# Performance work log

Measured on AMD Instinct MI355X. Metric: run time of the kernel, lower is better.

## Reference

```python
import jax, jax.numpy as jnp
import numpy as np

H = 1024


def _linear(x, W, b):
    # torch nn.Linear: y = x @ W.T + b
    return jnp.einsum('...i,oi->...o', x, W) + b


def setup_inputs() -> dict:
    key = jax.random.key(0)
    ks = jax.random.split(key, 10)
    s = 1.0 / np.sqrt(H)
    inp = {
        'p': jax.random.normal(ks[0], (8, 4096, H), dtype=jnp.float32),
        'x': jax.random.normal(ks[1], (8, 64, H), dtype=jnp.float32),
        'Wq': jax.random.uniform(ks[2], (H, H), jnp.float32, -s, s),
        'bq': jax.random.uniform(ks[3], (H,), jnp.float32, -s, s),
        'Wk': jax.random.uniform(ks[4], (H, H), jnp.float32, -s, s),
        'bk': jax.random.uniform(ks[5], (H,), jnp.float32, -s, s),
        'Wv': jax.random.uniform(ks[6], (H, H), jnp.float32, -s, s),
        'bv': jax.random.uniform(ks[7], (H,), jnp.float32, -s, s),
        'Wg': jax.random.uniform(ks[8], (1, 2 * H), jnp.float32, -s, s),
        'bg': jax.random.uniform(ks[9], (1,), jnp.float32, -s, s),
    }
    return inp


def reference(p, x, Wq, bq, Wk, bk, Wv, bv, Wg, bg):
    q = _linear(p, Wq, bq)            # (B, S, H)
    k = _linear(x, Wk, bk)            # (B, L, H)
    v = _linear(x, Wv, bv)            # (B, L, H)
    # NOTE: scale applied AFTER softmax, faithful to the original module
    scores = jax.nn.softmax(jnp.einsum('bsh,blh->bsl', q, k), axis=-1)
    scores = scores / jnp.sqrt(jnp.asarray(H, p.dtype))
    out = jnp.einsum('bsl,blh->bsh', scores, v) + p
    g = jax.nn.sigmoid(_linear(jnp.concatenate([out, p], axis=2), Wg, bg))  # (B,S,1)
    return g * out + (1.0 - g) * p
```

## Files before the change

kernel.cpp:

```cpp
#include <hip/hip_runtime.h>

#define H 1024
#define SEQ 4096

typedef float f32x4 __attribute__((ext_vector_type(4)));
typedef short s16x8 __attribute__((ext_vector_type(8)));
typedef unsigned short u16;
typedef u16 u16x4 __attribute__((ext_vector_type(4)));
typedef u16 u16x8 __attribute__((ext_vector_type(8)));

__device__ inline u16 f2bf(float f) {
  union { float f; unsigned u; } v; v.f = f;
  unsigned r = v.u + 0x7fffu + ((v.u >> 16) & 1u);
  return (u16)(r >> 16);
}
__device__ inline float bf2f(u16 b) {
  union { unsigned u; float f; } v; v.u = ((unsigned)b) << 16; return v.f;
}

__device__ __forceinline__ void cvt16(const float* __restrict__ src, u16* __restrict__ dst, int i) {
  const float4* s = reinterpret_cast<const float4*>(src) + (size_t)i * 4;
  float4 a = s[0], b = s[1], c = s[2], d = s[3];
  u16x8 lo, hi;
  lo[0]=f2bf(a.x); lo[1]=f2bf(a.y); lo[2]=f2bf(a.z); lo[3]=f2bf(a.w);
  lo[4]=f2bf(b.x); lo[5]=f2bf(b.y); lo[6]=f2bf(b.z); lo[7]=f2bf(b.w);
  hi[0]=f2bf(c.x); hi[1]=f2bf(c.y); hi[2]=f2bf(c.z); hi[3]=f2bf(c.w);
  hi[4]=f2bf(d.x); hi[5]=f2bf(d.y); hi[6]=f2bf(d.z); hi[7]=f2bf(d.w);
  u16x8* o = reinterpret_cast<u16x8*>(dst) + (size_t)i * 2;
  o[0] = lo; o[1] = hi;
}

__global__ __launch_bounds__(256) void prep_kernel(
    const float* __restrict__ Wq, const float* __restrict__ Wk,
    const float* __restrict__ Wv, const float* __restrict__ x,
    const float* __restrict__ Wg,
    u16* __restrict__ wqTb, u16* __restrict__ wkb, u16* __restrict__ wvb,
    u16* __restrict__ xb, float* __restrict__ wgs, float* __restrict__ zeros) {
  __shared__ u16 tls[64][65];
  int blk = blockIdx.x, t = threadIdx.x;
  if (blk < 256) {
    int ti = blk >> 4, tj = blk & 15;
    int lr = t >> 2, cq = (t & 3) * 16;
    const float* s = Wq + (size_t)(ti * 64 + lr) * H + tj * 64 + cq;
#pragma unroll
    for (int q = 0; q < 4; ++q) {
      float4 v = *reinterpret_cast<const float4*>(s + q * 4);
      tls[lr][cq + q * 4 + 0] = f2bf(v.x);
      tls[lr][cq + q * 4 + 1] = f2bf(v.y);
      tls[lr][cq + q * 4 + 2] = f2bf(v.z);
      tls[lr][cq + q * 4 + 3] = f2bf(v.w);
    }
    __syncthreads();
    u16x8 a, b2;
#pragma unroll
    for (int i = 0; i < 8; ++i) a[i] = tls[cq + i][lr];
#pragma unroll
    for (int i = 0; i < 8; ++i) b2[i] = tls[cq + 8 + i][lr];
    u16* d = wqTb + (size_t)(tj * 64 + lr) * H + ti * 64 + cq;
    *reinterpret_cast<u16x8*>(d) = a;
    *reinterpret_cast<u16x8*>(d + 8) = b2;
  } else if (blk < 512) {
    cvt16(Wk, wkb, (blk - 256) * 256 + t);
  } else if (blk < 768) {
    cvt16(Wv, wvb, (blk - 512) * 256 + t);
  } else if (blk < 896) {
    cvt16(x, xb, (blk - 768) * 256 + t);
  } else {
    int i = t * 4;
    float4 a = *reinterpret_cast<const float4*>(Wg + i);
    float4 b2 = *reinterpret_cast<const float4*>(Wg + H + i);
    float4 o; o.x=a.x+b2.x; o.y=a.y+b2.y; o.z=a.z+b2.z; o.w=a.w+b2.w;
    *reinterpret_cast<float4*>(wgs + i) = o;
    float4 z; z.x=0.f; z.y=0.f; z.z=0.f; z.w=0.f;
    *reinterpret_cast<float4*>(zeros + i) = z;
  }
}

__device__ __forceinline__ void gemm_body(const u16* __restrict__ A, const u16* __restrict__ W,
                                          const float* __restrict__ bias, u16* __restrict__ out,
                                          int mt, int nt, int omode, u16* sm) {
  int m0 = mt * 128, n0 = nt * 128;
  int t = threadIdx.x;
  int wave = t >> 6, lane = t & 63;
  int lane15 = lane & 15, lhi = lane >> 4;
  int wr = wave >> 1, wc = wave & 1;
  u16* a_sm = sm;
  u16* b_sm = sm + 8192;

  f32x4 acc[4][4];
#pragma unroll
  for (int mi = 0; mi < 4; ++mi)
#pragma unroll
    for (int ni = 0; ni < 4; ++ni) acc[mi][ni] = (f32x4)0.f;

  int rsel = wave * 32 + (lane >> 3);
  int csel = (lane & 7) * 8;
  const u16* Ab = A + (size_t)m0 * H + csel;
  const u16* Wb = W + (size_t)n0 * H + csel;

  for (int kt = 0; kt < 16; ++kt) {
    int kc = kt * 64;
#pragma unroll
    for (int j = 0; j < 4; ++j) {
      const u16* ga = Ab + (size_t)(rsel + j * 8) * H + kc;
      const u16* gb = Wb + (size_t)(rsel + j * 8) * H + kc;
      __builtin_amdgcn_global_load_lds((const __attribute__((address_space(1))) unsigned int*)ga,
                                       (__attribute__((address_space(3))) unsigned int*)&a_sm[wave * 2048 + j * 512],
                                       16, 0, 0);
      __builtin_amdgcn_global_load_lds((const __attribute__((address_space(1))) unsigned int*)gb,
                                       (__attribute__((address_space(3))) unsigned int*)&b_sm[wave * 2048 + j * 512],
                                       16, 0, 0);
    }
    __syncthreads();
#pragma unroll
    for (int ks = 0; ks < 2; ++ks) {
      s16x8 af[4], bfr[4];
#pragma unroll
      for (int mi = 0; mi < 4; ++mi)
        af[mi] = *reinterpret_cast<const s16x8*>(&a_sm[(wr * 64 + mi * 16 + lane15) * 64 + ks * 32 + lhi * 8]);
#pragma unroll
      for (int ni = 0; ni < 4; ++ni)
        bfr[ni] = *reinterpret_cast<const s16x8*>(&b_sm[(wc * 64 + ni * 16 + lane15) * 64 + ks * 32 + lhi * 8]);
#pragma unroll
      for (int mi = 0; mi < 4; ++mi)
#pragma unroll
        for (int ni = 0; ni < 4; ++ni)
          acc[mi][ni] = __builtin_amdgcn_mfma_f32_16x16x32_bf16(af[mi], bfr[ni], acc[mi][ni], 0, 0, 0);
    }
    __syncthreads();
  }

  float bqv[4];
#pragma unroll
  for (int ni = 0; ni < 4; ++ni) bqv[ni] = bias[n0 + wc * 64 + ni * 16 + lane15];

  if (omode == 0) {
#pragma unroll
    for (int mi = 0; mi < 4; ++mi)
#pragma unroll
      for (int ni = 0; ni < 4; ++ni)
#pragma unroll
        for (int r = 0; r < 4; ++r)
          sm[(wr * 64 + mi * 16 + lhi * 4 + r) * 128 + wc * 64 + ni * 16 + lane15] =
              f2bf(acc[mi][ni][r] + bqv[ni]);
    __syncthreads();
#pragma unroll
    for (int i = 0; i < 4; ++i) {
      int lin2 = i * 4096 + t * 16;
      int row = lin2 >> 7, col = lin2 & 127;
      u16x8 v0 = *reinterpret_cast<const u16x8*>(&sm[lin2]);
      u16x8 v1 = *reinterpret_cast<const u16x8*>(&sm[lin2 + 8]);
      u16* o = out + (size_t)(m0 + row) * H + n0 + col;
      *reinterpret_cast<u16x8*>(o) = v0;
      *reinterpret_cast<u16x8*>(o + 8) = v1;
    }
  } else {
#pragma unroll
    for (int mi = 0; mi < 4; ++mi)
#pragma unroll
      for (int ni = 0; ni < 4; ++ni) {
        int col = n0 + wc * 64 + ni * 16 + lane15;
#pragma unroll
        for (int r = 0; r < 4; ++r) {
          int row = m0 + wr * 64 + mi * 16 + lhi * 4 + r;
          out[((size_t)(row >> 6) * H + col) * 64 + (row & 63)] = f2bf(acc[mi][ni][r] + bqv[ni]);
        }
      }
  }
}

__global__ __launch_bounds__(256) void kv1_kernel(const u16* __restrict__ xb,
                                                  const u16* __restrict__ wkb, const u16* __restrict__ wvb,
                                                  const float* __restrict__ bk, const float* __restrict__ bv,
                                                  u16* __restrict__ kbf, u16* __restrict__ vTb) {
  __shared__ __align__(16) u16 sm[128 * 128];
  int sel = blockIdx.x >> 5;
  int bid = blockIdx.x & 31;
  if (sel == 0)
    gemm_body(xb, wkb, bk, kbf, bid >> 3, bid & 7, 0, sm);
  else
    gemm_body(xb, wvb, bv, vTb, bid >> 3, bid & 7, 2, sm);
}

__global__ __launch_bounds__(256) void kv2_kernel(const u16* __restrict__ kbf,
                                                  const u16* __restrict__ wqTb,
                                                  const float* __restrict__ zeros,
                                                  u16* __restrict__ ktb,
                                                  const u16* __restrict__ vTb,
                                                  const float* __restrict__ Wg,
                                                  const float* __restrict__ bq,
                                                  float* __restrict__ vg, float* __restrict__ bqk) {
  if (blockIdx.x < 32) {
    __shared__ __align__(16) u16 sm[128 * 128];
    gemm_body(kbf, wqTb, zeros, ktb, blockIdx.x >> 3, blockIdx.x & 7, 0, sm);
  } else {
    __shared__ float bq_s[H];
    __shared__ float partial[4][64];
    int b = blockIdx.x - 32, t = threadIdx.x;
    *reinterpret_cast<float4*>(&bq_s[t * 4]) = *reinterpret_cast<const float4*>(bq + t * 4);
    int l = t & 63, part = t >> 6;
    float s = 0.f;
    const u16* vtp = vTb + ((size_t)b * H + part * 256) * 64 + l;
    for (int h = 0; h < 256; ++h) s += bf2f(vtp[h * 64]) * Wg[part * 256 + h];
    partial[part][l] = s;
    __syncthreads();
    if (t < 64) vg[b * 64 + t] = partial[0][t] + partial[1][t] + partial[2][t] + partial[3][t];
    int row = t >> 2, qp = t & 3;
    const u16* kr = kbf + ((size_t)b * 64 + row) * H + qp * 256;
    float sb = 0.f;
    for (int j = 0; j < 256; j += 8) {
      u16x8 v8 = *reinterpret_cast<const u16x8*>(kr + j);
      const float* bqp = &bq_s[qp * 256 + j];
#pragma unroll
      for (int i2 = 0; i2 < 8; ++i2) sb += bf2f(v8[i2]) * bqp[i2];
    }
    sb += __shfl_xor(sb, 1);
    sb += __shfl_xor(sb, 2);
    if (qp == 0) bqk[b * 64 + row] = sb;
  }
}

__global__ __launch_bounds__(128, 2) void attn_kernel(
    const float* __restrict__ p, const u16* __restrict__ ktb,
    const u16* __restrict__ vT, const float* __restrict__ wgs,
    const float* __restrict__ vg, const float* __restrict__ bqk,
    const float* __restrict__ bg, float* __restrict__ out) {
  int t = threadIdx.x;
  int orig = blockIdx.x;
  int lin = (orig & 7) * 128 + (orig >> 3);
  int b = lin >> 7, st = lin & 127;
  size_t gm0 = (size_t)b * SEQ + (size_t)st * 32;
  int wave = t >> 6, lane = t & 63, lane15 = lane & 15, lhi = lane >> 4;

  __shared__ __align__(16) u16 kbuf[3][64 * 64];
  __shared__ __align__(16) u16 pbuf[2][32 * 64];
  __shared__ float wgs_l[H];
  __shared__ float g_l[32], vg_l[64], bq_l[64], pg_l[32];

  *reinterpret_cast<float4*>(&wgs_l[t * 8]) = *reinterpret_cast<const float4*>(wgs + t * 8);
  *reinterpret_cast<float4*>(&wgs_l[t * 8 + 4]) = *reinterpret_cast<const float4*>(wgs + t * 8 + 4);
  if (t < 64) { vg_l[t] = vg[b * 64 + t]; bq_l[t] = bqk[b * 64 + t]; }

  const u16* kb = ktb + (size_t)b * 64 * H;
  int ar = t >> 2, aq = t & 3;
  int awz = (ar & 7) << 3;
  const float* prow = p + (gm0 + ar) * H + aq * 16;
  float pgs = 0.f;

#define KSTAGE(buf, kc)                                                                   \
  {                                                                                       \
    _Pragma("unroll")                                                                     \
    for (int j = 0; j < 4; ++j) {                                                         \
      int row_ = j * 16 + wave * 8 + (lane >> 3);                                         \
      int off_ = (kc) + (((lane & 7) * 8) ^ ((row_ & 7) << 3));                           \
      __builtin_amdgcn_global_load_lds(                                                   \
          (const __attribute__((address_space(1))) unsigned int*)(kb + (size_t)row_ * H + off_), \
          (__attribute__((address_space(3))) unsigned int*)(&kbuf[buf][j * 1024 + wave * 512]),  \
          16, 0, 0);                                                                      \
    }                                                                                     \
  }

#define CVT_WRITE(buf, R, kc)                                                             \
  {                                                                                       \
    const float* w_ = &wgs_l[(kc) + aq * 16];                                             \
    pgs += R[0].x*w_[0]+R[0].y*w_[1]+R[0].z*w_[2]+R[0].w*w_[3]                            \
         + R[1].x*w_[4]+R[1].y*w_[5]+R[1].z*w_[6]+R[1].w*w_[7]                            \
         + R[2].x*w_[8]+R[2].y*w_[9]+R[2].z*w_[10]+R[2].w*w_[11]                          \
         + R[3].x*w_[12]+R[3].y*w_[13]+R[3].z*w_[14]+R[3].w*w_[15];                       \
    u16x8 o0_, o1_;                                                                       \
    o0_[0]=f2bf(R[0].x); o0_[1]=f2bf(R[0].y); o0_[2]=f2bf(R[0].z); o0_[3]=f2bf(R[0].w);   \
    o0_[4]=f2bf(R[1].x); o0_[5]=f2bf(R[1].y); o0_[6]=f2bf(R[1].z); o0_[7]=f2bf(R[1].w);   \
    o1_[0]=f2bf(R[2].x); o1_[1]=f2bf(R[2].y); o1_[2]=f2bf(R[2].z); o1_[3]=f2bf(R[2].w);   \
    o1_[4]=f2bf(R[3].x); o1_[5]=f2bf(R[3].y); o1_[6]=f2bf(R[3].z); o1_[7]=f2bf(R[3].w);   \
    *reinterpret_cast<u16x8*>(&pbuf[buf][ar * 64 + ((aq * 16) ^ awz)]) = o0_;             \
    *reinterpret_cast<u16x8*>(&pbuf[buf][ar * 64 + ((aq * 16 + 8) ^ awz)]) = o1_;         \
  }

#define PLOAD(R, kc)                                                                      \
  {                                                                                       \
    const float* pr_ = prow + (kc);                                                       \
    R[0] = *reinterpret_cast<const float4*>(pr_);                                         \
    R[1] = *reinterpret_cast<const float4*>(pr_ + 4);                                     \
    R[2] = *reinterpret_cast<const float4*>(pr_ + 8);                                     \
    R[3] = *reinterpret_cast<const float4*>(pr_ + 12);                                    \
  }

  float4 rA[4], rB[4], rC[4];
  KSTAGE(0, 0);
  KSTAGE(1, 64);
  PLOAD(rA, 0);
  PLOAD(rB, 64);
  PLOAD(rC, 128);
  __syncthreads();
  CVT_WRITE(0, rA, 0);
  PLOAD(rA, 192);

  f32x4 sacc[4];
#pragma unroll
  for (int ni = 0; ni < 4; ++ni) sacc[ni] = (f32x4)0.f;
  int aswz = (lane15 & 7) << 3;

  for (int kt = 0; kt < 16; ++kt) {
    int cur3 = kt % 3, cur2 = kt & 1;
    if (kt < 14) KSTAGE((kt + 2) % 3, (kt + 2) * 64);
    __builtin_amdgcn_sched_barrier(0);
    if (kt < 15) {
      int sel = (kt + 1) % 3;
      if (sel == 0)      { CVT_WRITE(cur2 ^ 1, rA, (kt + 1) * 64); if (kt < 12) PLOAD(rA, (kt + 4) * 64); }
      else if (sel == 1) { CVT_WRITE(cur2 ^ 1, rB, (kt + 1) * 64); if (kt < 12) PLOAD(rB, (kt + 4) * 64); }
      else               { CVT_WRITE(cur2 ^ 1, rC, (kt + 1) * 64); if (kt < 12) PLOAD(rC, (kt + 4) * 64); }
    }
#pragma unroll
    for (int ks2 = 0; ks2 < 2; ++ks2) {
      int col = ks2 * 32 + lhi * 8;
      s16x8 ap = *reinterpret_cast<const s16x8*>(&pbuf[cur2][(wave * 16 + lane15) * 64 + (col ^ aswz)]);
#pragma unroll
      for (int ni = 0; ni < 4; ++ni) {
        int brow = ni * 16 + lane15;
        s16x8 bk8 = *reinterpret_cast<const s16x8*>(&kbuf[cur3][brow * 64 + (col ^ ((brow & 7) << 3))]);
        sacc[ni] = __builtin_amdgcn_mfma_f32_16x16x32_bf16(ap, bk8, sacc[ni], 0, 0, 0);
      }
    }
    if (kt <= 11) {
      asm volatile("s_waitcnt vmcnt(12)" ::: "memory");
    } else if (kt == 12) {
      asm volatile("s_waitcnt vmcnt(8)" ::: "memory");
    } else {
      asm volatile("s_waitcnt vmcnt(0)" ::: "memory");
    }
    __builtin_amdgcn_s_barrier();
    asm volatile("" ::: "memory");
  }

  pgs += __shfl_xor(pgs, 1);
  pgs += __shfl_xor(pgs, 2);
  if (aq == 0) pg_l[ar] = pgs;
  __syncthreads();

  u16* P_lds = &pbuf[0][0];
  {
    float vgl[4], bql[4];
#pragma unroll
    for (int ni = 0; ni < 4; ++ni) { vgl[ni] = vg_l[ni * 16 + lane15]; bql[ni] = bq_l[ni * 16 + lane15]; }
    float bg0 = bg[0];
#pragma unroll
    for (int r = 0; r < 4; ++r) {
      int row = wave * 16 + lhi * 4 + r;
      float sv[4];
#pragma unroll
      for (int ni = 0; ni < 4; ++ni) sv[ni] = sacc[ni][r] + bql[ni];
      float mx = fmaxf(fmaxf(sv[0], sv[1]), fmaxf(sv[2], sv[3]));
      mx = fmaxf(mx, __shfl_xor(mx, 1));
      mx = fmaxf(mx, __shfl_xor(mx, 2));
      mx = fmaxf(mx, __shfl_xor(mx, 4));
      mx = fmaxf(mx, __shfl_xor(mx, 8));
      float sum = 0.f;
#pragma unroll
      for (int ni = 0; ni < 4; ++ni) {
        float e = __expf(sv[ni] - mx);
        sv[ni] = e;
        sum += e;
      }
      sum += __shfl_xor(sum, 1);
      sum += __shfl_xor(sum, 2);
      sum += __shfl_xor(sum, 4);
      sum += __shfl_xor(sum, 8);
      float inv = 1.f / (32.f * sum);
      float gl = 0.f;
#pragma unroll
      for (int ni = 0; ni < 4; ++ni) {
        float pv = sv[ni] * inv;
        P_lds[row * 72 + ni * 16 + lane15] = f2bf(pv);
        gl += pv * vgl[ni];
      }
      gl += __shfl_xor(gl, 1);
      gl += __shfl_xor(gl, 2);
      gl += __shfl_xor(gl, 4);
      gl += __shfl_xor(gl, 8);
      if (lane15 == 0) {
        float logit = gl + pg_l[row] + bg0;
        g_l[row] = 1.f / (1.f + __expf(-logit));
      }
    }
  }
  __syncthreads();

  {
    s16x8 pa[2][2];
#pragma unroll
    for (int mi = 0; mi < 2; ++mi)
#pragma unroll
      for (int ks = 0; ks < 2; ++ks)
        pa[mi][ks] = *reinterpret_cast<const s16x8*>(&P_lds[(mi * 16 + lane15) * 72 + ks * 32 + lhi * 8]);
    const u16* vb = vT + (size_t)b * H * 64;
    float* sc = reinterpret_cast<float*>(&kbuf[0][0]) + wave * 2048;
    for (int hc = 0; hc < 8; ++hc) {
      int hbase = wave * 512 + hc * 64;
      f32x4 acc[2][4];
#pragma unroll
      for (int mi = 0; mi < 2; ++mi)
#pragma unroll
        for (int ni = 0; ni < 4; ++ni) acc[mi][ni] = (f32x4)0.f;
#pragma unroll
      for (int ks = 0; ks < 2; ++ks) {
        s16x8 bv8[4];
#pragma unroll
        for (int ni = 0; ni < 4; ++ni)
          bv8[ni] = *reinterpret_cast<const s16x8*>(vb + (size_t)(hbase + ni * 16 + lane15) * 64 + ks * 32 + lhi * 8);
#pragma unroll
        for (int mi = 0; mi < 2; ++mi)
#pragma unroll
          for (int ni = 0; ni < 4; ++ni)
            acc[mi][ni] = __builtin_amdgcn_mfma_f32_16x16x32_bf16(pa[mi][ks], bv8[ni], acc[mi][ni], 0, 0, 0);
      }
      int swz = (lhi & 1) << 4;
#pragma unroll
      for (int mi = 0; mi < 2; ++mi)
#pragma unroll
        for (int ni = 0; ni < 4; ++ni)
#pragma unroll
          for (int r = 0; r < 4; ++r)
            sc[(mi * 16 + lhi * 4 + r) * 64 + ((ni * 16 + lane15) ^ swz)] = acc[mi][ni][r];
      asm volatile("s_waitcnt lgkmcnt(0)" ::: "memory");
      __builtin_amdgcn_sched_barrier(0);
#pragma unroll
      for (int ii = 0; ii < 8; ++ii) {
        int flat4 = ii * 64 + lane;
        int lrow = flat4 >> 4;
        int c4 = flat4 & 15;
        int scol = (c4 * 4) ^ (((lrow >> 2) & 1) << 4);
        f32x4 a = *reinterpret_cast<const f32x4*>(&sc[lrow * 64 + scol]);
        size_t grow = gm0 + lrow;
        float g = g_l[lrow];
        float4 pr4 = *reinterpret_cast<const float4*>(&p[grow * H + hbase + c4 * 4]);
        f32x4 o;
        o[0] = pr4.x + g * a[0];
        o[1] = pr4.y + g * a[1];
        o[2] = pr4.z + g * a[2];
        o[3] = pr4.w + g * a[3];
        *reinterpret_cast<f32x4*>(&out[grow * H + hbase + c4 * 4]) = o;
      }
      asm volatile("s_waitcnt lgkmcnt(0)" ::: "memory");
    }
  }
#undef KSTAGE
#undef CVT_WRITE
#undef PLOAD
}

extern "C" void kernel_launch(void* const* d_in, const int* in_sizes, int n_in,
                              void* d_out, int out_size, void* d_ws, size_t ws_size,
                              hipStream_t stream) {
  const float* p  = (const float*)d_in[0];
  const float* x  = (const float*)d_in[1];
  const float* Wq = (const float*)d_in[2];
  const float* bq = (const float*)d_in[3];
  const float* Wk = (const float*)d_in[4];
  const float* bk = (const float*)d_in[5];
  const float* Wv = (const float*)d_in[6];
  const float* bv = (const float*)d_in[7];
  const float* Wg = (const float*)d_in[8];
  const float* bg = (const float*)d_in[9];
  float* out = (float*)d_out;

  char* ws = (char*)d_ws;
  u16* wqTb    = (u16*)(ws);
  u16* wkb     = (u16*)(ws + 2097152);
  u16* wvb     = (u16*)(ws + 4194304);
  u16* xb      = (u16*)(ws + 6291456);
  u16* kbf     = (u16*)(ws + 7340032);
  u16* ktb     = (u16*)(ws + 8388608);
  u16* vTb     = (u16*)(ws + 9437184);
  float* wgs   = (float*)(ws + 10485760);
  float* zeros = (float*)(ws + 10489856);
  float* vg    = (float*)(ws + 10493952);
  float* bqk   = (float*)(ws + 10498048);

  prep_kernel<<<897, 256, 0, stream>>>(Wq, Wk, Wv, x, Wg, wqTb, wkb, wvb, xb, wgs, zeros);
  kv1_kernel<<<64, 256, 0, stream>>>(xb, wkb, wvb, bk, bv, kbf, vTb);
  kv2_kernel<<<40, 256, 0, stream>>>(kbf, wqTb, zeros, ktb, vTb, Wg, bq, vg, bqk);
  attn_kernel<<<1024, 128, 0, stream>>>(p, ktb, vTb, wgs, vg, bqk, bg, out);
}
```

Measured before the change: 124.0 us.

## Use 256-thread attention blocks with 2x2 wave tiling and max-free softmax

```diff
diff --git a/kernel.cpp b/kernel.cpp
--- a/kernel.cpp
+++ b/kernel.cpp
@@ -220,7 +220,7 @@
   }
 }
 
-__global__ __launch_bounds__(128, 2) void attn_kernel(
+__global__ __launch_bounds__(256, 4) void attn_kernel(
     const float* __restrict__ p, const u16* __restrict__ ktb,
     const u16* __restrict__ vT, const float* __restrict__ wgs,
     const float* __restrict__ vg, const float* __restrict__ bqk,
@@ -231,49 +231,47 @@
   int b = lin >> 7, st = lin & 127;
   size_t gm0 = (size_t)b * SEQ + (size_t)st * 32;
   int wave = t >> 6, lane = t & 63, lane15 = lane & 15, lhi = lane >> 4;
-
-  __shared__ __align__(16) u16 kbuf[3][64 * 64];
-  __shared__ __align__(16) u16 pbuf[2][32 * 64];
+  int wr = wave & 1, wc2 = wave >> 1;
+
+  __shared__ __align__(16) u16 smem_u[16384];
   __shared__ float wgs_l[H];
-  __shared__ float g_l[32], vg_l[64], bq_l[64], pg_l[32];
-
-  *reinterpret_cast<float4*>(&wgs_l[t * 8]) = *reinterpret_cast<const float4*>(wgs + t * 8);
-  *reinterpret_cast<float4*>(&wgs_l[t * 8 + 4]) = *reinterpret_cast<const float4*>(wgs + t * 8 + 4);
+  __shared__ float sum_l[2][32], gv_l[2][32];
+  __shared__ float gs_l[32], pg_l[32], vg_l[64], bq_l[64];
+
+#define KBUF(bb) (&smem_u[(bb) * 4096])
+#define PBUF(bb) (&smem_u[12288 + (bb) * 2048])
+
+  *reinterpret_cast<float4*>(&wgs_l[t * 4]) = *reinterpret_cast<const float4*>(wgs + t * 4);
   if (t < 64) { vg_l[t] = vg[b * 64 + t]; bq_l[t] = bqk[b * 64 + t]; }
 
   const u16* kb = ktb + (size_t)b * 64 * H;
-  int ar = t >> 2, aq = t & 3;
+  int ar = t >> 3, aq = t & 7;
   int awz = (ar & 7) << 3;
-  const float* prow = p + (gm0 + ar) * H + aq * 16;
+  const float* prow = p + (gm0 + ar) * H + aq * 8;
   float pgs = 0.f;
 
 #define KSTAGE(buf, kc)                                                                   \
   {                                                                                       \
     _Pragma("unroll")                                                                     \
-    for (int j = 0; j < 4; ++j) {                                                         \
-      int row_ = j * 16 + wave * 8 + (lane >> 3);                                         \
+    for (int j = 0; j < 2; ++j) {                                                         \
+      int row_ = j * 32 + wave * 8 + (lane >> 3);                                         \
       int off_ = (kc) + (((lane & 7) * 8) ^ ((row_ & 7) << 3));                           \
       __builtin_amdgcn_global_load_lds(                                                   \
           (const __attribute__((address_space(1))) unsigned int*)(kb + (size_t)row_ * H + off_), \
-          (__attribute__((address_space(3))) unsigned int*)(&kbuf[buf][j * 1024 + wave * 512]),  \
+          (__attribute__((address_space(3))) unsigned int*)(KBUF(buf) + j * 2048 + wave * 512),  \
           16, 0, 0);                                                                      \
     }                                                                                     \
   }
 
 #define CVT_WRITE(buf, R, kc)                                                             \
   {                                                                                       \
-    const float* w_ = &wgs_l[(kc) + aq * 16];                                             \
+    const float* w_ = &wgs_l[(kc) + aq * 8];                                              \
     pgs += R[0].x*w_[0]+R[0].y*w_[1]+R[0].z*w_[2]+R[0].w*w_[3]                            \
-         + R[1].x*w_[4]+R[1].y*w_[5]+R[1].z*w_[6]+R[1].w*w_[7]                            \
-         + R[2].x*w_[8]+R[2].y*w_[9]+R[2].z*w_[10]+R[2].w*w_[11]                          \
-         + R[3].x*w_[12]+R[3].y*w_[13]+R[3].z*w_[14]+R[3].w*w_[15];                       \
-    u16x8 o0_, o1_;                                                                       \
-    o0_[0]=f2bf(R[0].x); o0_[1]=f2bf(R[0].y); o0_[2]=f2bf(R[0].z); o0_[3]=f2bf(R[0].w);   \
-    o0_[4]=f2bf(R[1].x); o0_[5]=f2bf(R[1].y); o0_[6]=f2bf(R[1].z); o0_[7]=f2bf(R[1].w);   \
-    o1_[0]=f2bf(R[2].x); o1_[1]=f2bf(R[2].y); o1_[2]=f2bf(R[2].z); o1_[3]=f2bf(R[2].w);   \
-    o1_[4]=f2bf(R[3].x); o1_[5]=f2bf(R[3].y); o1_[6]=f2bf(R[3].z); o1_[7]=f2bf(R[3].w);   \
-    *reinterpret_cast<u16x8*>(&pbuf[buf][ar * 64 + ((aq * 16) ^ awz)]) = o0_;             \
-    *reinterpret_cast<u16x8*>(&pbuf[buf][ar * 64 + ((aq * 16 + 8) ^ awz)]) = o1_;         \
+         + R[1].x*w_[4]+R[1].y*w_[5]+R[1].z*w_[6]+R[1].w*w_[7];                           \
+    u16x8 o_;                                                                             \
+    o_[0]=f2bf(R[0].x); o_[1]=f2bf(R[0].y); o_[2]=f2bf(R[0].z); o_[3]=f2bf(R[0].w);       \
+    o_[4]=f2bf(R[1].x); o_[5]=f2bf(R[1].y); o_[6]=f2bf(R[1].z); o_[7]=f2bf(R[1].w);       \
+    *reinterpret_cast<u16x8*>(&PBUF(buf)[ar * 64 + ((aq * 8) ^ awz)]) = o_;               \
   }
 
 #define PLOAD(R, kc)                                                                      \
@@ -281,11 +279,9 @@
     const float* pr_ = prow + (kc);                                                       \
     R[0] = *reinterpret_cast<const float4*>(pr_);                                         \
     R[1] = *reinterpret_cast<const float4*>(pr_ + 4);                                     \
-    R[2] = *reinterpret_cast<const float4*>(pr_ + 8);                                     \
-    R[3] = *reinterpret_cast<const float4*>(pr_ + 12);                                    \
-  }
-
-  float4 rA[4], rB[4], rC[4];
+  }
+
+  float4 rA[2], rB[2], rC[2];
   KSTAGE(0, 0);
   KSTAGE(1, 64);
   PLOAD(rA, 0);
@@ -294,10 +290,13 @@
   __syncthreads();
   CVT_WRITE(0, rA, 0);
   PLOAD(rA, 192);
-
-  f32x4 sacc[4];
-#pragma unroll
-  for (int ni = 0; ni < 4; ++ni) sacc[ni] = (f32x4)0.f;
+  asm volatile("s_waitcnt lgkmcnt(0)" ::: "memory");
+  __builtin_amdgcn_s_barrier();
+  asm volatile("" ::: "memory");
+
+  f32x4 sacc[2];
+  sacc[0] = (f32x4)0.f;
+  sacc[1] = (f32x4)0.f;
   int aswz = (lane15 & 7) << 3;
 
   for (int kt = 0; kt < 16; ++kt) {
@@ -313,20 +312,22 @@
 #pragma unroll
     for (int ks2 = 0; ks2 < 2; ++ks2) {
       int col = ks2 * 32 + lhi * 8;
-      s16x8 ap = *reinterpret_cast<const s16x8*>(&pbuf[cur2][(wave * 16 + lane15) * 64 + (col ^ aswz)]);
-#pragma unroll
-      for (int ni = 0; ni < 4; ++ni) {
-        int brow = ni * 16 + lane15;
-        s16x8 bk8 = *reinterpret_cast<const s16x8*>(&kbuf[cur3][brow * 64 + (col ^ ((brow & 7) << 3))]);
+      s16x8 ap = *reinterpret_cast<const s16x8*>(&PBUF(cur2)[(wr * 16 + lane15) * 64 + (col ^ aswz)]);
+#pragma unroll
+      for (int ni = 0; ni < 2; ++ni) {
+        int brow = wc2 * 32 + ni * 16 + lane15;
+        s16x8 bk8 = *reinterpret_cast<const s16x8*>(&KBUF(cur3)[brow * 64 + (col ^ ((brow & 7) << 3))]);
         sacc[ni] = __builtin_amdgcn_mfma_f32_16x16x32_bf16(ap, bk8, sacc[ni], 0, 0, 0);
       }
     }
     if (kt <= 11) {
-      asm volatile("s_waitcnt vmcnt(12)" ::: "memory");
+      asm volatile("s_waitcnt vmcnt(6) lgkmcnt(0)" ::: "memory");
     } else if (kt == 12) {
-      asm volatile("s_waitcnt vmcnt(8)" ::: "memory");
+      asm volatile("s_waitcnt vmcnt(4) lgkmcnt(0)" ::: "memory");
+    } else if (kt == 13) {
+      asm volatile("s_waitcnt vmcnt(2) lgkmcnt(0)" ::: "memory");
     } else {
-      asm volatile("s_waitcnt vmcnt(0)" ::: "memory");
+      asm volatile("s_waitcnt vmcnt(0) lgkmcnt(0)" ::: "memory");
     }
     __builtin_amdgcn_s_barrier();
     asm volatile("" ::: "memory");
@@ -334,68 +335,58 @@
 
   pgs += __shfl_xor(pgs, 1);
   pgs += __shfl_xor(pgs, 2);
+  pgs += __shfl_xor(pgs, 4);
   if (aq == 0) pg_l[ar] = pgs;
+
+  u16* P_lds = PBUF(0);
+  {
+    float vgl[2], bql[2];
+#pragma unroll
+    for (int ni = 0; ni < 2; ++ni) {
+      int c = wc2 * 32 + ni * 16 + lane15;
+      vgl[ni] = vg_l[c];
+      bql[ni] = bq_l[c];
+    }
+#pragma unroll
+    for (int r = 0; r < 4; ++r) {
+      int row = wr * 16 + lhi * 4 + r;
+      float e0 = __expf(sacc[0][r] + bql[0]);
+      float e1 = __expf(sacc[1][r] + bql[1]);
+      float se = e0 + e1;
+      float sv = e0 * vgl[0] + e1 * vgl[1];
+      se += __shfl_xor(se, 1); se += __shfl_xor(se, 2);
+      se += __shfl_xor(se, 4); se += __shfl_xor(se, 8);
+      sv += __shfl_xor(sv, 1); sv += __shfl_xor(sv, 2);
+      sv += __shfl_xor(sv, 4); sv += __shfl_xor(sv, 8);
+      P_lds[row * 72 + wc2 * 32 + lane15] = f2bf(e0);
+      P_lds[row * 72 + wc2 * 32 + 16 + lane15] = f2bf(e1);
+      if (lane15 == 0) { sum_l[wc2][row] = se; gv_l[wc2][row] = sv; }
+    }
+  }
   __syncthreads();
 
-  u16* P_lds = &pbuf[0][0];
+  if (t < 32) {
+    float ssum = sum_l[0][t] + sum_l[1][t];
+    float inv = 1.f / (32.f * ssum);
+    float logit = (gv_l[0][t] + gv_l[1][t]) * inv + pg_l[t] + bg[0];
+    gs_l[t] = inv / (1.f + __expf(-logit));
+  }
+
+  s16x8 pa[2][2];
+#pragma unroll
+  for (int mi = 0; mi < 2; ++mi)
+#pragma unroll
+    for (int ks = 0; ks < 2; ++ks)
+      pa[mi][ks] = *reinterpret_cast<const s16x8*>(&P_lds[(mi * 16 + lane15) * 72 + ks * 32 + lhi * 8]);
+  asm volatile("s_waitcnt lgkmcnt(0)" ::: "memory");
+  __syncthreads();
+
   {
-    float vgl[4], bql[4];
-#pragma unroll
-    for (int ni = 0; ni < 4; ++ni) { vgl[ni] = vg_l[ni * 16 + lane15]; bql[ni] = bq_l[ni * 16 + lane15]; }
-    float bg0 = bg[0];
-#pragma unroll
-    for (int r = 0; r < 4; ++r) {
-      int row = wave * 16 + lhi * 4 + r;
-      float sv[4];
-#pragma unroll
-      for (int ni = 0; ni < 4; ++ni) sv[ni] = sacc[ni][r] + bql[ni];
-      float mx = fmaxf(fmaxf(sv[0], sv[1]), fmaxf(sv[2], sv[3]));
-      mx = fmaxf(mx, __shfl_xor(mx, 1));
-      mx = fmaxf(mx, __shfl_xor(mx, 2));
-      mx = fmaxf(mx, __shfl_xor(mx, 4));
-      mx = fmaxf(mx, __shfl_xor(mx, 8));
-      float sum = 0.f;
-#pragma unroll
-      for (int ni = 0; ni < 4; ++ni) {
-        float e = __expf(sv[ni] - mx);
-        sv[ni] = e;
-        sum += e;
-      }
-      sum += __shfl_xor(sum, 1);
-      sum += __shfl_xor(sum, 2);
-      sum += __shfl_xor(sum, 4);
-      sum += __shfl_xor(sum, 8);
-      float inv = 1.f / (32.f * sum);
-      float gl = 0.f;
-#pragma unroll
-      for (int ni = 0; ni < 4; ++ni) {
-        float pv = sv[ni] * inv;
-        P_lds[row * 72 + ni * 16 + lane15] = f2bf(pv);
-        gl += pv * vgl[ni];
-      }
-      gl += __shfl_xor(gl, 1);
-      gl += __shfl_xor(gl, 2);
-      gl += __shfl_xor(gl, 4);
-      gl += __shfl_xor(gl, 8);
-      if (lane15 == 0) {
-        float logit = gl + pg_l[row] + bg0;
-        g_l[row] = 1.f / (1.f + __expf(-logit));
-      }
-    }
-  }
-  __syncthreads();
-
-  {
-    s16x8 pa[2][2];
-#pragma unroll
-    for (int mi = 0; mi < 2; ++mi)
-#pragma unroll
-      for (int ks = 0; ks < 2; ++ks)
-        pa[mi][ks] = *reinterpret_cast<const s16x8*>(&P_lds[(mi * 16 + lane15) * 72 + ks * 32 + lhi * 8]);
     const u16* vb = vT + (size_t)b * H * 64;
-    float* sc = reinterpret_cast<float*>(&kbuf[0][0]) + wave * 2048;
-    for (int hc = 0; hc < 8; ++hc) {
-      int hbase = wave * 512 + hc * 64;
+    float* sc = reinterpret_cast<float*>(&smem_u[0]) + wave * 2048;
+#pragma unroll
+    for (int hcc = 0; hcc < 4; ++hcc) {
+      int hbase = wave * 256 + hcc * 64;
       f32x4 acc[2][4];
 #pragma unroll
       for (int mi = 0; mi < 2; ++mi)
@@ -431,13 +422,13 @@
         int scol = (c4 * 4) ^ (((lrow >> 2) & 1) << 4);
         f32x4 a = *reinterpret_cast<const f32x4*>(&sc[lrow * 64 + scol]);
         size_t grow = gm0 + lrow;
-        float g = g_l[lrow];
+        float f = gs_l[lrow];
         float4 pr4 = *reinterpret_cast<const float4*>(&p[grow * H + hbase + c4 * 4]);
         f32x4 o;
-        o[0] = pr4.x + g * a[0];
-        o[1] = pr4.y + g * a[1];
-        o[2] = pr4.z + g * a[2];
-        o[3] = pr4.w + g * a[3];
+        o[0] = pr4.x + f * a[0];
+        o[1] = pr4.y + f * a[1];
+        o[2] = pr4.z + f * a[2];
+        o[3] = pr4.w + f * a[3];
         *reinterpret_cast<f32x4*>(&out[grow * H + hbase + c4 * 4]) = o;
       }
       asm volatile("s_waitcnt lgkmcnt(0)" ::: "memory");
@@ -446,6 +437,8 @@
 #undef KSTAGE
 #undef CVT_WRITE
 #undef PLOAD
+#undef KBUF
+#undef PBUF
 }
 
 extern "C" void kernel_launch(void* const* d_in, const int* in_sizes, int n_in,
@@ -479,5 +472,5 @@
   prep_kernel<<<897, 256, 0, stream>>>(Wq, Wk, Wv, x, Wg, wqTb, wkb, wvb, xb, wgs, zeros);
   kv1_kernel<<<64, 256, 0, stream>>>(xb, wkb, wvb, bk, bv, kbf, vTb);
   kv2_kernel<<<40, 256, 0, stream>>>(kbf, wqTb, zeros, ktb, vTb, Wg, bq, vg, bqk);
-  attn_kernel<<<1024, 128, 0, stream>>>(p, ktb, vTb, wgs, vg, bqk, bg, out);
-}
+  attn_kernel<<<1024, 256, 0, stream>>>(p, ktb, vTb, wgs, vg, bqk, bg, out);
+}
```

Result: faster. 120.3 us (-3.0%).
